# Performance work log

Measured on AMD Instinct MI355X. Metric: run time of the kernel, lower is better.

## Reference

```python
import jax, jax.numpy as jnp
import numpy as np

V, D, H, DFF, L = 32000, 256, 4, 1024, 4
B, T = 2, 2048
DK = D // H
EPS = 1e-5


def setup_inputs() -> dict:
    key = jax.random.key(0)
    ks = jax.random.split(key, 8)
    s = 0.02
    return {
        "tokens": jax.random.randint(ks[0], (B, T), 0, V),
        "embed": jax.random.normal(ks[1], (V, D), jnp.float32) * s,
        "qkv_w": jax.random.normal(ks[2], (L, 3 * D, D), jnp.float32) * s,
        "qkv_b": jnp.zeros((L, 3 * D), jnp.float32),
        "fc_w": jax.random.normal(ks[3], (L, D, D), jnp.float32) * s,
        "fc_b": jnp.zeros((L, D), jnp.float32),
        "ln1_s": jnp.ones((L, D), jnp.float32),
        "ln1_b": jnp.zeros((L, D), jnp.float32),
        "w1": jax.random.normal(ks[4], (L, DFF, D), jnp.float32) * s,
        "b1": jnp.zeros((L, DFF), jnp.float32),
        "w2": jax.random.normal(ks[5], (L, D, DFF), jnp.float32) * s,
        "b2": jnp.zeros((L, D), jnp.float32),
        "ln2_s": jnp.ones((L, D), jnp.float32),
        "ln2_b": jnp.zeros((L, D), jnp.float32),
        "lnf_s": jnp.ones((D,), jnp.float32),
        "lnf_b": jnp.zeros((D,), jnp.float32),
        "out_w": jax.random.normal(ks[6], (V, D), jnp.float32) * s,
        "out_b": jnp.zeros((V,), jnp.float32),
    }


def _layernorm(x, s, b):
    mu = jnp.mean(x, axis=-1, keepdims=True)
    var = jnp.mean(jnp.square(x - mu), axis=-1, keepdims=True)
    return (x - mu) * jax.lax.rsqrt(var + EPS) * s + b


def _pos_encoding(t, d):
    pos = jnp.arange(t, dtype=jnp.float32)[:, None]
    div = jnp.exp(jnp.arange(0, d, 2, dtype=jnp.float32) * (-np.log(10000.0) / d))
    pe = jnp.zeros((t, d), jnp.float32)
    pe = pe.at[:, 0::2].set(jnp.sin(pos * div))
    pe = pe.at[:, 1::2].set(jnp.cos(pos * div))
    return pe


def reference(tokens, embed, qkv_w, qkv_b, fc_w, fc_b, ln1_s, ln1_b,
              w1, b1, w2, b2, ln2_s, ln2_b, lnf_s, lnf_b, out_w, out_b):
    b, t = tokens.shape
    x = embed[tokens] + _pos_encoding(t, D)[None]  # [B,T,D]
    causal = jnp.tril(jnp.ones((t, t), bool))
    scale = 1.0 / np.sqrt(DK)
    for l in range(L):
        # --- attention ---
        qkv = jnp.einsum('btd,ed->bte', x, qkv_w[l]) + qkv_b[l]  # [B,T,3D]
        qkv = qkv.reshape(b, t, 3, H, DK)
        q, k, v = qkv[:, :, 0], qkv[:, :, 1], qkv[:, :, 2]  # [B,T,H,DK]
        scores = jnp.einsum('bqhd,bkhd->bhqk', q, k) * scale
        scores = jnp.where(causal, scores, -jnp.inf)
        attn = jax.nn.softmax(scores, axis=-1)
        o = jnp.einsum('bhqk,bkhd->bqhd', attn, v).reshape(b, t, D)
        o = jnp.einsum('btd,ed->bte', o, fc_w[l]) + fc_b[l]
        x = _layernorm(x + o, ln1_s[l], ln1_b[l])
        # --- feed-forward ---
        h = jax.nn.relu(jnp.einsum('btd,fd->btf', x, w1[l]) + b1[l])
        f = jnp.einsum('btf,df->btd', h, w2[l]) + b2[l]
        x = _layernorm(x + f, ln2_s[l], ln2_b[l])
    x = _layernorm(x, lnf_s, lnf_b)
    logits = jnp.einsum('btd,vd->btv', x, out_w) + out_b
    return logits
```

## Files before the change

kernel.cpp:

```cpp
#include <hip/hip_runtime.h>
#include <math.h>

typedef __attribute__((ext_vector_type(8))) short bf16x8;
typedef __attribute__((ext_vector_type(4))) float f32x4;
typedef __attribute__((ext_vector_type(4))) unsigned int u32x4;
typedef __attribute__((ext_vector_type(4))) unsigned short u16x4;

static constexpr int Tn = 2048;
static constexpr int Dm = 256;
static constexpr int NHn = 4;
static constexpr int Ln = 4;
static constexpr int DFFn = 1024;
static constexpr int Vn = 32000;
static constexpr int BTn = 4096;

__device__ __forceinline__ unsigned short f2bf(float f) {
  unsigned int u = __float_as_uint(f);
  u += 0x7fffu + ((u >> 16) & 1u);
  return (unsigned short)(u >> 16);
}

__global__ __launch_bounds__(256) void cvt_f2bf(const float* __restrict__ in,
                                                unsigned short* __restrict__ out, int n) {
  int i = (blockIdx.x * 256 + threadIdx.x) * 4;
  if (i >= n) return;
  float4 v = *reinterpret_cast<const float4*>(in + i);
  u16x4 o;
  o[0] = f2bf(v.x); o[1] = f2bf(v.y); o[2] = f2bf(v.z); o[3] = f2bf(v.w);
  *reinterpret_cast<u16x4*>(out + i) = o;
}

__global__ __launch_bounds__(256) void embed_pos(const int* __restrict__ tokens,
                                                 const float* __restrict__ emb,
                                                 float* __restrict__ xf,
                                                 unsigned short* __restrict__ xb) {
  int idx = blockIdx.x * 256 + threadIdx.x;
  int bt = idx >> 8, d = idx & 255;
  int t = bt & (Tn - 1);
  int tok = tokens[bt];
  float v = emb[(size_t)tok * Dm + d];
  int i2 = d & ~1;
  float dv = expf((float)i2 * (-0.03597789207803249f));
  float arg = (float)t * dv;
  float pe = (d & 1) ? cosf(arg) : sinf(arg);
  float x = v + pe;
  xf[idx] = x;
  xb[idx] = f2bf(x);
}

__global__ __launch_bounds__(256) void add_ln(const float* __restrict__ addend,
                                              const float* __restrict__ gam,
                                              const float* __restrict__ bet,
                                              float* __restrict__ xf,
                                              unsigned short* __restrict__ xb) {
  int row = blockIdx.x, d = threadIdx.x;
  __shared__ float red[8];
  size_t off = (size_t)row * Dm + d;
  float u = xf[off];
  if (addend) u += addend[off];
  float tsum = u;
  #pragma unroll
  for (int o = 32; o > 0; o >>= 1) tsum += __shfl_xor(tsum, o);
  int w = d >> 6, lane = d & 63;
  if (lane == 0) red[w] = tsum;
  __syncthreads();
  float mean = (red[0] + red[1] + red[2] + red[3]) * (1.f / 256.f);
  float df = u - mean;
  float vsum = df * df;
  #pragma unroll
  for (int o = 32; o > 0; o >>= 1) vsum += __shfl_xor(vsum, o);
  if (lane == 0) red[4 + w] = vsum;
  __syncthreads();
  float var = (red[4] + red[5] + red[6] + red[7]) * (1.f / 256.f);
  float y = df * rsqrtf(var + 1e-5f) * gam[d] + bet[d];
  xf[off] = y;
  xb[off] = f2bf(y);
}

__global__ __launch_bounds__(256) void attn_mfma(const unsigned short* __restrict__ qkv,
                                                 unsigned short* __restrict__ ob) {
  int bh = blockIdx.y;
  int b = bh >> 2, h = bh & 3;
  int q0 = blockIdx.x * 64;
  int tid = threadIdx.x;
  int lane = tid & 63, w = tid >> 6;
  int l15 = lane & 15, quad = lane >> 4;

  __shared__ __align__(16) unsigned short Ps[4][16 * 64];
  __shared__ __align__(16) unsigned short Vt[64 * 64];

  const size_t rowQ = (size_t)(b * Tn + q0 + w * 16 + l15) * 768 + h * 64 + quad * 8;
  bf16x8 aq0 = *reinterpret_cast<const bf16x8*>(qkv + rowQ);
  bf16x8 aq1 = *reinterpret_cast<const bf16x8*>(qkv + rowQ + 32);

  float m_i[4], l_i[4];
  f32x4 oacc[4];
  #pragma unroll
  for (int i = 0; i < 4; i++) { m_i[i] = -INFINITY; l_i[i] = 0.f; oacc[i] = (f32x4){0.f, 0.f, 0.f, 0.f}; }

  for (int jt = 0; jt <= blockIdx.x; jt++) {
    int j0 = jt * 64;
    __syncthreads();
    {
      int kv = tid & 63, g = tid >> 6;
      const unsigned short* vsrc = qkv + (size_t)(b * Tn + j0 + kv) * 768 + 512 + h * 64 + g * 16;
      bf16x8 v0 = *reinterpret_cast<const bf16x8*>(vsrc);
      bf16x8 v1 = *reinterpret_cast<const bf16x8*>(vsrc + 8);
      char* vb = (char*)Vt;
      #pragma unroll
      for (int j = 0; j < 8; j++) {
        int dk = g * 16 + j;
        *(unsigned short*)(vb + (((dk * 128 + kv * 2)) ^ ((dk & 7) << 4))) = (unsigned short)v0[j];
      }
      #pragma unroll
      for (int j = 0; j < 8; j++) {
        int dk = g * 16 + 8 + j;
        *(unsigned short*)(vb + (((dk * 128 + kv * 2)) ^ ((dk & 7) << 4))) = (unsigned short)v1[j];
      }
    }
    __syncthreads();

    f32x4 sc[4];
    const size_t rowK = (size_t)(b * Tn + j0 + l15) * 768 + 256 + h * 64 + quad * 8;
    #pragma unroll
    for (int f = 0; f < 4; f++) {
      bf16x8 bk0 = *reinterpret_cast<const bf16x8*>(qkv + rowK + (size_t)f * 16 * 768);
      bf16x8 bk1 = *reinterpret_cast<const bf16x8*>(qkv + rowK + (size_t)f * 16 * 768 + 32);
      f32x4 a = (f32x4){0.f, 0.f, 0.f, 0.f};
      a = __builtin_amdgcn_mfma_f32_16x16x32_bf16(aq0, bk0, a, 0, 0, 0);
      a = __builtin_amdgcn_mfma_f32_16x16x32_bf16(aq1, bk1, a, 0, 0, 0);
      sc[f] = a;
    }

    bool diag = (jt == blockIdx.x);
    float alpha[4];
    #pragma unroll
    for (int rr = 0; rr < 4; rr++) {
      int qg = q0 + w * 16 + quad * 4 + rr;
      float sv[4];
      #pragma unroll
      for (int f = 0; f < 4; f++) {
        sv[f] = sc[f][rr] * 0.125f;
        if (diag && (j0 + f * 16 + l15 > qg)) sv[f] = -INFINITY;
      }
      float mx = fmaxf(fmaxf(sv[0], sv[1]), fmaxf(sv[2], sv[3]));
      #pragma unroll
      for (int o = 8; o > 0; o >>= 1) mx = fmaxf(mx, __shfl_xor(mx, o));
      float mnew = fmaxf(m_i[rr], mx);
      float p[4], ps = 0.f;
      #pragma unroll
      for (int f = 0; f < 4; f++) { p[f] = __expf(sv[f] - mnew); ps += p[f]; }
      #pragma unroll
      for (int o = 8; o > 0; o >>= 1) ps += __shfl_xor(ps, o);
      alpha[rr] = __expf(m_i[rr] - mnew);
      l_i[rr] = l_i[rr] * alpha[rr] + ps;
      m_i[rr] = mnew;
      int q = quad * 4 + rr;
      char* pb = (char*)Ps[w];
      #pragma unroll
      for (int f = 0; f < 4; f++)
        *(unsigned short*)(pb + (((q * 128 + (f * 16 + l15) * 2)) ^ ((q & 7) << 4))) = f2bf(p[f]);
    }

    #pragma unroll
    for (int ni = 0; ni < 4; ni++)
      #pragma unroll
      for (int rr = 0; rr < 4; rr++) oacc[ni][rr] *= alpha[rr];

    bf16x8 pa[2];
    {
      char* pb = (char*)Ps[w];
      #pragma unroll
      for (int kc = 0; kc < 2; kc++)
        pa[kc] = *reinterpret_cast<const bf16x8*>(
            pb + (((l15 * 128 + kc * 64 + quad * 16)) ^ ((l15 & 7) << 4)));
    }
    char* vb = (char*)Vt;
    #pragma unroll
    for (int ni = 0; ni < 4; ni++) {
      int dk = ni * 16 + l15;
      #pragma unroll
      for (int kc = 0; kc < 2; kc++) {
        bf16x8 bv = *reinterpret_cast<const bf16x8*>(
            vb + (((dk * 128 + kc * 64 + quad * 16)) ^ ((dk & 7) << 4)));
        oacc[ni] = __builtin_amdgcn_mfma_f32_16x16x32_bf16(pa[kc], bv, oacc[ni], 0, 0, 0);
      }
    }
  }

  #pragma unroll
  for (int ni = 0; ni < 4; ni++) {
    #pragma unroll
    for (int rr = 0; rr < 4; rr++) {
      int q = q0 + w * 16 + quad * 4 + rr;
      float o = oacc[ni][rr] / l_i[rr];
      ob[(size_t)(b * Tn + q) * Dm + h * 64 + ni * 16 + l15] = f2bf(o);
    }
  }
}

template <int EPI>
__global__ __launch_bounds__(256) void gemm_bt(const unsigned short* __restrict__ A,
                                               const unsigned short* __restrict__ W,
                                               const float* __restrict__ bias,
                                               float* __restrict__ Cf,
                                               unsigned short* __restrict__ Cb,
                                               int M, int N, int K) {
  constexpr int LDA = 40;
  __shared__ __align__(16) unsigned short As[128 * LDA];
  __shared__ __align__(16) unsigned short Bs[128 * LDA];
  int tid = threadIdx.x;
  int lane = tid & 63, w = tid >> 6;
  int wm = (w >> 1) * 64, wn = (w & 1) * 64;
  int r = lane & 15, quad = lane >> 4;
  int m0 = blockIdx.y * 128, n0 = blockIdx.x * 128;
  f32x4 acc[4][4];
  #pragma unroll
  for (int i = 0; i < 4; i++)
    #pragma unroll
    for (int j = 0; j < 4; j++) acc[i][j] = (f32x4){0.f, 0.f, 0.f, 0.f};
  int row0 = tid >> 2, s4 = (tid & 3) * 8;
  for (int k0 = 0; k0 < K; k0 += 32) {
    __syncthreads();
    #pragma unroll
    for (int i = 0; i < 2; i++) {
      int row = row0 + i * 64;
      u32x4 va = *reinterpret_cast<const u32x4*>(A + (size_t)(m0 + row) * K + k0 + s4);
      *reinterpret_cast<u32x4*>(&As[row * LDA + s4]) = va;
      u32x4 vb = *reinterpret_cast<const u32x4*>(W + (size_t)(n0 + row) * K + k0 + s4);
      *reinterpret_cast<u32x4*>(&Bs[row * LDA + s4]) = vb;
    }
    __syncthreads();
    bf16x8 af[4], bfr[4];
    #pragma unroll
    for (int mi = 0; mi < 4; mi++)
      af[mi] = *reinterpret_cast<const bf16x8*>(&As[(wm + mi * 16 + r) * LDA + quad * 8]);
    #pragma unroll
    for (int ni = 0; ni < 4; ni++)
      bfr[ni] = *reinterpret_cast<const bf16x8*>(&Bs[(wn + ni * 16 + r) * LDA + quad * 8]);
    #pragma unroll
    for (int mi = 0; mi < 4; mi++)
      #pragma unroll
      for (int ni = 0; ni < 4; ni++)
        acc[mi][ni] = __builtin_amdgcn_mfma_f32_16x16x32_bf16(af[mi], bfr[ni], acc[mi][ni], 0, 0, 0);
  }
  #pragma unroll
  for (int mi = 0; mi < 4; mi++) {
    #pragma unroll
    for (int ni = 0; ni < 4; ni++) {
      int n = n0 + wn + ni * 16 + r;
      float bv = bias[n];
      #pragma unroll
      for (int rr = 0; rr < 4; rr++) {
        int m = m0 + wm + mi * 16 + quad * 4 + rr;
        float v = acc[mi][ni][rr] + bv;
        if (EPI == 0) {
          Cf[(size_t)m * N + n] = v;
        } else if (EPI == 1) {
          Cb[(size_t)m * N + n] = f2bf(fmaxf(v, 0.f));
        } else {
          Cb[(size_t)m * N + n] = f2bf(v);
        }
      }
    }
  }
}

extern "C" void kernel_launch(void* const* d_in, const int* in_sizes, int n_in,
                              void* d_out, int out_size, void* d_ws, size_t ws_size,
                              hipStream_t stream) {
  (void)in_sizes; (void)n_in; (void)out_size; (void)ws_size;
  const int* tokens = (const int*)d_in[0];
  const float* emb = (const float*)d_in[1];
  const float* qkv_w = (const float*)d_in[2];
  const float* qkv_b = (const float*)d_in[3];
  const float* fc_w = (const float*)d_in[4];
  const float* fc_b = (const float*)d_in[5];
  const float* ln1_s = (const float*)d_in[6];
  const float* ln1_b = (const float*)d_in[7];
  const float* w1 = (const float*)d_in[8];
  const float* b1 = (const float*)d_in[9];
  const float* w2 = (const float*)d_in[10];
  const float* b2 = (const float*)d_in[11];
  const float* ln2_s = (const float*)d_in[12];
  const float* ln2_b = (const float*)d_in[13];
  const float* lnf_s = (const float*)d_in[14];
  const float* lnf_b = (const float*)d_in[15];
  const float* out_w = (const float*)d_in[16];
  const float* out_b = (const float*)d_in[17];
  float* logits = (float*)d_out;

  char* p = (char*)d_ws;
  auto carve = [&](size_t bytes) {
    char* r = p;
    p += (bytes + 255) & ~(size_t)255;
    return r;
  };
  float* xf = (float*)carve((size_t)BTn * Dm * 4);
  unsigned short* xb = (unsigned short*)carve((size_t)BTn * Dm * 2);
  unsigned short* qkvb = (unsigned short*)carve((size_t)BTn * 768 * 2);
  unsigned short* obb = (unsigned short*)carve((size_t)BTn * Dm * 2);
  float* of = (float*)carve((size_t)BTn * Dm * 4);
  unsigned short* hb = (unsigned short*)carve((size_t)BTn * DFFn * 2);
  float* ff = (float*)carve((size_t)BTn * Dm * 4);
  unsigned short* wqkvb = (unsigned short*)carve((size_t)Ln * 768 * Dm * 2);
  unsigned short* wfcb = (unsigned short*)carve((size_t)Ln * Dm * Dm * 2);
  unsigned short* w1b = (unsigned short*)carve((size_t)Ln * DFFn * Dm * 2);
  unsigned short* w2b = (unsigned short*)carve((size_t)Ln * Dm * DFFn * 2);
  unsigned short* outwb = (unsigned short*)carve((size_t)Vn * Dm * 2);

  auto cvt = [&](const float* src, unsigned short* dst, int n) {
    cvt_f2bf<<<dim3((n / 4 + 255) / 256), dim3(256), 0, stream>>>(src, dst, n);
  };
  cvt(qkv_w, wqkvb, Ln * 768 * Dm);
  cvt(fc_w, wfcb, Ln * Dm * Dm);
  cvt(w1, w1b, Ln * DFFn * Dm);
  cvt(w2, w2b, Ln * Dm * DFFn);
  cvt(out_w, outwb, Vn * Dm);

  embed_pos<<<dim3(BTn), dim3(256), 0, stream>>>(tokens, emb, xf, xb);

  for (int l = 0; l < Ln; l++) {
    gemm_bt<2><<<dim3(768 / 128, BTn / 128), dim3(256), 0, stream>>>(
        xb, wqkvb + (size_t)l * 768 * Dm, qkv_b + l * 768, nullptr, qkvb, BTn, 768, Dm);
    attn_mfma<<<dim3(Tn / 64, 2 * NHn), dim3(256), 0, stream>>>(qkvb, obb);
    gemm_bt<0><<<dim3(Dm / 128, BTn / 128), dim3(256), 0, stream>>>(
        obb, wfcb + (size_t)l * Dm * Dm, fc_b + l * Dm, of, nullptr, BTn, Dm, Dm);
    add_ln<<<dim3(BTn), dim3(256), 0, stream>>>(of, ln1_s + l * Dm, ln1_b + l * Dm, xf, xb);
    gemm_bt<1><<<dim3(DFFn / 128, BTn / 128), dim3(256), 0, stream>>>(
        xb, w1b + (size_t)l * DFFn * Dm, b1 + l * DFFn, nullptr, hb, BTn, DFFn, Dm);
    gemm_bt<0><<<dim3(Dm / 128, BTn / 128), dim3(256), 0, stream>>>(
        hb, w2b + (size_t)l * Dm * DFFn, b2 + l * Dm, ff, nullptr, BTn, Dm, DFFn);
    add_ln<<<dim3(BTn), dim3(256), 0, stream>>>(ff, ln2_s + l * Dm, ln2_b + l * Dm, xf, xb);
  }
  add_ln<<<dim3(BTn), dim3(256), 0, stream>>>(nullptr, lnf_s, lnf_b, xf, xb);

  gemm_bt<0><<<dim3(Vn / 128, BTn / 128), dim3(256), 0, stream>>>(
      xb, outwb, out_b, logits, nullptr, BTn, Vn, Dm);
}
```

Before: 1.273 ms.

## Use direct global-to-LDS loads, XCD-aware tile remap, and smaller M tiles

The GEMM now loads A and W tiles straight into LDS with global_load_lds 16-byte transfers instead of going through registers, and drops the padded layout. Workgroups are remapped so that consecutive tiles land on the same XCD, and the grid is reordered with M-fastest ordering. Narrow-N GEMMs use 64-row tiles to raise workgroup counts, and attention blocks are remapped across XCDs as well. The unpadded 32-element LDS rows may cause bank conflicts on fragment reads.

Result: no change. 1.253 ms (-1.6%).

```diff
diff --git a/kernel.cpp b/kernel.cpp
--- a/kernel.cpp
+++ b/kernel.cpp
@@ -18,6 +18,11 @@
   unsigned int u = __float_as_uint(f);
   u += 0x7fffu + ((u >> 16) & 1u);
   return (unsigned short)(u >> 16);
+}
+
+__device__ __forceinline__ void gld_lds16(const unsigned short* g, unsigned short* l) {
+  __builtin_amdgcn_global_load_lds((const __attribute__((address_space(1))) unsigned int*)g,
+                                   (__attribute__((address_space(3))) unsigned int*)l, 16, 0, 0);
 }
 
 __global__ __launch_bounds__(256) void cvt_f2bf(const float* __restrict__ in,
@@ -79,9 +84,11 @@
 
 __global__ __launch_bounds__(256) void attn_mfma(const unsigned short* __restrict__ qkv,
                                                  unsigned short* __restrict__ ob) {
-  int bh = blockIdx.y;
+  int lin = blockIdx.y * gridDim.x + blockIdx.x;
+  int wg = (lin & 7) * 32 + (lin >> 3);
+  int qb = wg & 31, bh = wg >> 5;
   int b = bh >> 2, h = bh & 3;
-  int q0 = blockIdx.x * 64;
+  int q0 = qb * 64;
   int tid = threadIdx.x;
   int lane = tid & 63, w = tid >> 6;
   int l15 = lane & 15, quad = lane >> 4;
@@ -98,7 +105,7 @@
   #pragma unroll
   for (int i = 0; i < 4; i++) { m_i[i] = -INFINITY; l_i[i] = 0.f; oacc[i] = (f32x4){0.f, 0.f, 0.f, 0.f}; }
 
-  for (int jt = 0; jt <= blockIdx.x; jt++) {
+  for (int jt = 0; jt <= qb; jt++) {
     int j0 = jt * 64;
     __syncthreads();
     {
@@ -132,7 +139,7 @@
       sc[f] = a;
     }
 
-    bool diag = (jt == blockIdx.x);
+    bool diag = (jt == qb);
     float alpha[4];
     #pragma unroll
     for (int rr = 0; rr < 4; rr++) {
@@ -155,11 +162,11 @@
       alpha[rr] = __expf(m_i[rr] - mnew);
       l_i[rr] = l_i[rr] * alpha[rr] + ps;
       m_i[rr] = mnew;
-      int q = quad * 4 + rr;
+      int qq = quad * 4 + rr;
       char* pb = (char*)Ps[w];
       #pragma unroll
       for (int f = 0; f < 4; f++)
-        *(unsigned short*)(pb + (((q * 128 + (f * 16 + l15) * 2)) ^ ((q & 7) << 4))) = f2bf(p[f]);
+        *(unsigned short*)(pb + (((qq * 128 + (f * 16 + l15) * 2)) ^ ((qq & 7) << 4))) = f2bf(p[f]);
     }
 
     #pragma unroll
@@ -192,60 +199,72 @@
   for (int ni = 0; ni < 4; ni++) {
     #pragma unroll
     for (int rr = 0; rr < 4; rr++) {
-      int q = q0 + w * 16 + quad * 4 + rr;
+      int qg = q0 + w * 16 + quad * 4 + rr;
       float o = oacc[ni][rr] / l_i[rr];
-      ob[(size_t)(b * Tn + q) * Dm + h * 64 + ni * 16 + l15] = f2bf(o);
-    }
-  }
-}
-
-template <int EPI>
+      ob[(size_t)(b * Tn + qg) * Dm + h * 64 + ni * 16 + l15] = f2bf(o);
+    }
+  }
+}
+
+template <int BM, int EPI>
 __global__ __launch_bounds__(256) void gemm_bt(const unsigned short* __restrict__ A,
                                                const unsigned short* __restrict__ W,
                                                const float* __restrict__ bias,
                                                float* __restrict__ Cf,
                                                unsigned short* __restrict__ Cb,
                                                int M, int N, int K) {
-  constexpr int LDA = 40;
-  __shared__ __align__(16) unsigned short As[128 * LDA];
-  __shared__ __align__(16) unsigned short Bs[128 * LDA];
+  constexpr int MI = BM / 32;
+  __shared__ __align__(16) unsigned short As[BM * 32];
+  __shared__ __align__(16) unsigned short Bs[128 * 32];
   int tid = threadIdx.x;
   int lane = tid & 63, w = tid >> 6;
-  int wm = (w >> 1) * 64, wn = (w & 1) * 64;
+  int wm = (w >> 1) * (BM / 2), wn = (w & 1) * 64;
   int r = lane & 15, quad = lane >> 4;
-  int m0 = blockIdx.y * 128, n0 = blockIdx.x * 128;
-  f32x4 acc[4][4];
-  #pragma unroll
-  for (int i = 0; i < 4; i++)
+
+  int nwg = gridDim.x * gridDim.y;
+  int lin = blockIdx.y * gridDim.x + blockIdx.x;
+  int xcd = lin & 7, pos = lin >> 3;
+  int qch = nwg >> 3, rch = nwg & 7;
+  int wg = (xcd < rch ? xcd * (qch + 1) : rch * (qch + 1) + (xcd - rch) * qch) + pos;
+  int m0 = (wg % gridDim.x) * BM;
+  int n0 = (wg / gridDim.x) * 128;
+
+  f32x4 acc[MI][4];
+  #pragma unroll
+  for (int i = 0; i < MI; i++)
     #pragma unroll
     for (int j = 0; j < 4; j++) acc[i][j] = (f32x4){0.f, 0.f, 0.f, 0.f};
-  int row0 = tid >> 2, s4 = (tid & 3) * 8;
+
+  int lrow = lane >> 2;
+  int lcol = (lane & 3) * 8;
   for (int k0 = 0; k0 < K; k0 += 32) {
     __syncthreads();
     #pragma unroll
+    for (int i = 0; i < BM / 64; i++) {
+      int rowA = i * 64 + w * 16;
+      gld_lds16(A + (size_t)(m0 + rowA + lrow) * K + k0 + lcol, &As[rowA * 32]);
+    }
+    #pragma unroll
     for (int i = 0; i < 2; i++) {
-      int row = row0 + i * 64;
-      u32x4 va = *reinterpret_cast<const u32x4*>(A + (size_t)(m0 + row) * K + k0 + s4);
-      *reinterpret_cast<u32x4*>(&As[row * LDA + s4]) = va;
-      u32x4 vb = *reinterpret_cast<const u32x4*>(W + (size_t)(n0 + row) * K + k0 + s4);
-      *reinterpret_cast<u32x4*>(&Bs[row * LDA + s4]) = vb;
+      int rowB = i * 64 + w * 16;
+      gld_lds16(W + (size_t)(n0 + rowB + lrow) * K + k0 + lcol, &Bs[rowB * 32]);
     }
     __syncthreads();
-    bf16x8 af[4], bfr[4];
-    #pragma unroll
-    for (int mi = 0; mi < 4; mi++)
-      af[mi] = *reinterpret_cast<const bf16x8*>(&As[(wm + mi * 16 + r) * LDA + quad * 8]);
+    bf16x8 af[MI], bfr[4];
+    #pragma unroll
+    for (int mi = 0; mi < MI; mi++)
+      af[mi] = *reinterpret_cast<const bf16x8*>(&As[(wm + mi * 16 + r) * 32 + quad * 8]);
     #pragma unroll
     for (int ni = 0; ni < 4; ni++)
-      bfr[ni] = *reinterpret_cast<const bf16x8*>(&Bs[(wn + ni * 16 + r) * LDA + quad * 8]);
-    #pragma unroll
-    for (int mi = 0; mi < 4; mi++)
+      bfr[ni] = *reinterpret_cast<const bf16x8*>(&Bs[(wn + ni * 16 + r) * 32 + quad * 8]);
+    #pragma unroll
+    for (int mi = 0; mi < MI; mi++)
       #pragma unroll
       for (int ni = 0; ni < 4; ni++)
         acc[mi][ni] = __builtin_amdgcn_mfma_f32_16x16x32_bf16(af[mi], bfr[ni], acc[mi][ni], 0, 0, 0);
   }
   #pragma unroll
-  for (int mi = 0; mi < 4; mi++) {
+  for (int mi = 0; mi < MI; mi++) {
     #pragma unroll
     for (int ni = 0; ni < 4; ni++) {
       int n = n0 + wn + ni * 16 + r;
@@ -321,20 +340,20 @@
   embed_pos<<<dim3(BTn), dim3(256), 0, stream>>>(tokens, emb, xf, xb);
 
   for (int l = 0; l < Ln; l++) {
-    gemm_bt<2><<<dim3(768 / 128, BTn / 128), dim3(256), 0, stream>>>(
+    gemm_bt<64, 2><<<dim3(BTn / 64, 768 / 128), dim3(256), 0, stream>>>(
         xb, wqkvb + (size_t)l * 768 * Dm, qkv_b + l * 768, nullptr, qkvb, BTn, 768, Dm);
     attn_mfma<<<dim3(Tn / 64, 2 * NHn), dim3(256), 0, stream>>>(qkvb, obb);
-    gemm_bt<0><<<dim3(Dm / 128, BTn / 128), dim3(256), 0, stream>>>(
+    gemm_bt<64, 0><<<dim3(BTn / 64, Dm / 128), dim3(256), 0, stream>>>(
         obb, wfcb + (size_t)l * Dm * Dm, fc_b + l * Dm, of, nullptr, BTn, Dm, Dm);
     add_ln<<<dim3(BTn), dim3(256), 0, stream>>>(of, ln1_s + l * Dm, ln1_b + l * Dm, xf, xb);
-    gemm_bt<1><<<dim3(DFFn / 128, BTn / 128), dim3(256), 0, stream>>>(
+    gemm_bt<128, 1><<<dim3(BTn / 128, DFFn / 128), dim3(256), 0, stream>>>(
         xb, w1b + (size_t)l * DFFn * Dm, b1 + l * DFFn, nullptr, hb, BTn, DFFn, Dm);
-    gemm_bt<0><<<dim3(Dm / 128, BTn / 128), dim3(256), 0, stream>>>(
+    gemm_bt<64, 0><<<dim3(BTn / 64, Dm / 128), dim3(256), 0, stream>>>(
         hb, w2b + (size_t)l * Dm * DFFn, b2 + l * Dm, ff, nullptr, BTn, Dm, DFFn);
     add_ln<<<dim3(BTn), dim3(256), 0, stream>>>(ff, ln2_s + l * Dm, ln2_b + l * Dm, xf, xb);
   }
   add_ln<<<dim3(BTn), dim3(256), 0, stream>>>(nullptr, lnf_s, lnf_b, xf, xb);
 
-  gemm_bt<0><<<dim3(Vn / 128, BTn / 128), dim3(256), 0, stream>>>(
+  gemm_bt<128, 0><<<dim3(BTn / 128, Vn / 128), dim3(256), 0, stream>>>(
       xb, outwb, out_b, logits, nullptr, BTn, Vn, Dm);
 }
```
